# Kernel optimization log

Hardware: AMD Instinct MI355X
Metric: run time of the kernel (lower is better)

Reference implementation:

```python
import jax, jax.numpy as jnp
import numpy as np

N_ITEM_SRC = 100000
N_ITEM_DST = 50000
N_USER0 = 50000
N_USER1 = 25000
E_II = 800000
E_IU0 = 800000
E_IU1 = 400000
D_IN = 256
D_H = 256
D_OUT = 128


def setup_inputs() -> dict:
    key = jax.random.key(0)
    ks = jax.random.split(key, 16)
    f = jnp.float32
    s = 0.05  # weight init scale
    return {
        "x_item": jax.random.normal(ks[0], (N_ITEM_SRC, D_IN), f),
        "x_user": jax.random.normal(ks[1], (N_USER0, D_H), f),
        "src_ii": jax.random.randint(ks[2], (E_II,), 0, N_ITEM_SRC, jnp.int32),
        "dst_ii": jax.random.randint(ks[3], (E_II,), 0, N_ITEM_DST, jnp.int32),
        "src_iu0": jax.random.randint(ks[4], (E_IU0,), 0, N_ITEM_SRC, jnp.int32),
        "dst_iu0": jax.random.randint(ks[5], (E_IU0,), 0, N_USER0, jnp.int32),
        "src_iu1": jax.random.randint(ks[6], (E_IU1,), 0, N_ITEM_DST, jnp.int32),
        "dst_iu1": jax.random.randint(ks[7], (E_IU1,), 0, N_USER1, jnp.int32),
        "Wn1": jax.random.normal(ks[8], (D_IN, D_H), f) * s,
        "Ws1": jax.random.normal(ks[9], (D_IN, D_H), f) * s,
        "b1": jnp.zeros((D_H,), f),
        "Wn2": jax.random.normal(ks[10], (D_H, D_H), f) * s,
        "Ws2": jax.random.normal(ks[11], (D_H, D_H), f) * s,
        "b2": jnp.zeros((D_H,), f),
        "Wn3": jax.random.normal(ks[12], (D_H, D_H), f) * s,
        "Ws3": jax.random.normal(ks[13], (D_H, D_H), f) * s,
        "b3": jnp.zeros((D_H,), f),
        "Wlin": jax.random.normal(ks[14], (D_H, D_OUT), f) * s,
        "blin": jnp.zeros((D_OUT,), f),
        "n_item_dst": N_ITEM_DST,
        "n_user1": N_USER1,
    }


def _sage_mean(x_src, x_dst, src, dst, n_dst, Wn, Ws, b):
    """DGL SAGEConv('mean'): fc_self(x_dst) + fc_neigh(mean_{in-nbrs} x_src) + bias.
    Isolated dst nodes get zero neighbor contribution (clamp degree to 1)."""
    deg = jax.ops.segment_sum(jnp.ones(dst.shape, x_src.dtype), dst, num_segments=n_dst)
    agg = jax.ops.segment_sum(x_src[src], dst, num_segments=n_dst)  # [n_dst, d]
    agg = agg / jnp.maximum(deg, 1.0)[:, None]
    return x_dst @ Ws + agg @ Wn + b


def reference(x_item, x_user, src_ii, dst_ii, src_iu0, dst_iu0, src_iu1, dst_iu1,
              Wn1, Ws1, b1, Wn2, Ws2, b2, Wn3, Ws3, b3, Wlin, blin,
              n_item_dst, n_user1):
    # conv1: item->item (block: dst item feats are prefix of src item feats)
    item_x = jax.nn.relu(_sage_mean(x_item, x_item[:n_item_dst], src_ii, dst_ii,
                                    n_item_dst, Wn1, Ws1, b1))
    # conv2: item->user at hop 0
    user_x = jax.nn.relu(_sage_mean(x_item, x_user, src_iu0, dst_iu0,
                                    x_user.shape[0], Wn2, Ws2, b2))
    user_x = user_x[:n_user1]
    # conv3: item->user at hop 1
    user_x = jax.nn.relu(_sage_mean(item_x, user_x, src_iu1, dst_iu1,
                                    n_user1, Wn3, Ws3, b3))
    return user_x @ Wlin + blin
```

## Files before the change

### kernel.cpp

```cpp
#include <hip/hip_runtime.h>

#define D 256
#define NI_SRC 100000
#define NI_DST 50000
#define NU1 25000
#define EII 800000
#define EIU0 800000
#define EIU1 400000
#define DOUT 128
#define CAP 56
#define CSTRIDE 16

#define NB_BUCKET 512
#define NB_WCVT 1664
#define NB_CVT 12500
#define NGRP1 100000
#define NGRP2 100000
#define NGRP3 50000
#define NGRP 250000

typedef __bf16 bf16x8 __attribute__((ext_vector_type(8)));
typedef float f32x4 __attribute__((ext_vector_type(4)));

__device__ __forceinline__ unsigned short f2bf(float x) {
    unsigned u = __builtin_bit_cast(unsigned, x);
    u += 0x7FFFu + ((u >> 16) & 1u);
    return (unsigned short)(u >> 16);
}
__device__ __forceinline__ float bflo(unsigned u) { return __builtin_bit_cast(float, u << 16); }
__device__ __forceinline__ float bfhi(unsigned u) { return __builtin_bit_cast(float, u & 0xFFFF0000u); }

__device__ __forceinline__ void bucket8p(const int* __restrict__ src, const int* __restrict__ dst,
                                         int* __restrict__ cur, int* __restrict__ csr,
                                         int g, int dmax) {
    const int4 da = reinterpret_cast<const int4*>(dst)[g * 2];
    const int4 db = reinterpret_cast<const int4*>(dst)[g * 2 + 1];
    const int4 sa = reinterpret_cast<const int4*>(src)[g * 2];
    const int4 sb = reinterpret_cast<const int4*>(src)[g * 2 + 1];
    int d[8] = {da.x, da.y, da.z, da.w, db.x, db.y, db.z, db.w};
    int s[8] = {sa.x, sa.y, sa.z, sa.w, sb.x, sb.y, sb.z, sb.w};
    int p[8];
#pragma unroll
    for (int q = 0; q < 8; ++q)
        p[q] = (d[q] < dmax) ? atomicAdd(&cur[d[q] * CSTRIDE], 1) : CAP;
#pragma unroll
    for (int q = 0; q < 8; ++q)
        if (p[q] < CAP) csr[d[q] * CAP + p[q]] = s[q];
}

__global__ __launch_bounds__(256) void prep_kernel(
    const int* __restrict__ s1, const int* __restrict__ d1, int* __restrict__ c1, int* __restrict__ e1,
    const int* __restrict__ s2, const int* __restrict__ d2, int* __restrict__ c2, int* __restrict__ e2,
    const int* __restrict__ s3, const int* __restrict__ d3, int* __restrict__ c3, int* __restrict__ e3,
    const float* __restrict__ W0, const float* __restrict__ W1, const float* __restrict__ W2,
    const float* __restrict__ W3, const float* __restrict__ W4, const float* __restrict__ W5,
    const float* __restrict__ W6, unsigned short* __restrict__ wout,
    const float* __restrict__ xin, unsigned short* __restrict__ xout)
{
    int b = blockIdx.x;
    if (b < NB_BUCKET) {
        int t0 = b * 256 + threadIdx.x;
        for (int g = t0; g < NGRP; g += NB_BUCKET * 256) {
            if (g < NGRP1) bucket8p(s1, d1, c1, e1, g, NI_DST);
            else if (g < NGRP1 + NGRP2) bucket8p(s2, d2, c2, e2, g - NGRP1, NU1);
            else bucket8p(s3, d3, c3, e3, g - NGRP1 - NGRP2, NU1);
        }
    } else if (b < NB_BUCKET + NB_WCVT) {
        int t = (b - NB_BUCKET) * 256 + threadIdx.x;
        const float* W; int NN; int base;
        if (t < 393216) {
            int w = t >> 16; base = w << 16;
            W = (w == 0) ? W0 : (w == 1) ? W1 : (w == 2) ? W2 : (w == 3) ? W3 : (w == 4) ? W4 : W5;
            NN = 256;
        } else { base = 393216; W = W6; NN = 128; }
        int i = t - base;
        int n = i >> 8, k = i & 255;
        wout[t] = f2bf(W[(size_t)k * NN + n]);
    } else {
        long i = (long)(b - NB_BUCKET - NB_WCVT) * 256 + threadIdx.x;
        const float4 f1 = *reinterpret_cast<const float4*>(xin + i * 8);
        const float4 f2 = *reinterpret_cast<const float4*>(xin + i * 8 + 4);
        uint4 v;
        v.x = f2bf(f1.x) | ((unsigned)f2bf(f1.y) << 16);
        v.y = f2bf(f1.z) | ((unsigned)f2bf(f1.w) << 16);
        v.z = f2bf(f2.x) | ((unsigned)f2bf(f2.y) << 16);
        v.w = f2bf(f2.z) | ((unsigned)f2bf(f2.w) << 16);
        *reinterpret_cast<uint4*>(xout + i * 8) = v;
    }
}

__device__ __forceinline__ void gather_seg(const unsigned short* __restrict__ X,
                                           const int* __restrict__ csr,
                                           const int* __restrict__ cnt,
                                           unsigned short* __restrict__ out,
                                           int nrows, int wid, int lane) {
    if (wid >= nrows) return;
    int c = min(cnt[wid * CSTRIDE], CAP);
    const int len0 = (c + 1) >> 1;
    const int half = lane >> 5;
    const int l32 = lane & 31;
    const int myc = half ? (c - len0) : len0;
    int myid = (l32 < myc) ? csr[wid * CAP + half * len0 + l32] : 0;
    float acc[8] = {};
    for (int t = 0; t < len0; ++t) {
        int sid = __shfl(myid, t + half * 32, 64);
        if (t < myc) {
            const uint4 v = *reinterpret_cast<const uint4*>(X + (size_t)sid * D + l32 * 8);
            acc[0] += bflo(v.x); acc[1] += bfhi(v.x);
            acc[2] += bflo(v.y); acc[3] += bfhi(v.y);
            acc[4] += bflo(v.z); acc[5] += bfhi(v.z);
            acc[6] += bflo(v.w); acc[7] += bfhi(v.w);
        }
    }
#pragma unroll
    for (int q = 0; q < 8; ++q) acc[q] += __shfl_xor(acc[q], 32, 64);
    if (half == 0) {
        float r = 1.0f / fmaxf((float)c, 1.0f);
        uint4 o;
        o.x = f2bf(acc[0] * r) | ((unsigned)f2bf(acc[1] * r) << 16);
        o.y = f2bf(acc[2] * r) | ((unsigned)f2bf(acc[3] * r) << 16);
        o.z = f2bf(acc[4] * r) | ((unsigned)f2bf(acc[5] * r) << 16);
        o.w = f2bf(acc[6] * r) | ((unsigned)f2bf(acc[7] * r) << 16);
        *reinterpret_cast<uint4*>(out + (size_t)wid * D + l32 * 8) = o;
    }
}

__global__ __launch_bounds__(256) void gather_cap(const unsigned short* __restrict__ X,
                                                  const int* __restrict__ csr,
                                                  const int* __restrict__ cnt,
                                                  unsigned short* __restrict__ out, int nrows) {
    int wid = (blockIdx.x * blockDim.x + threadIdx.x) >> 6;
    gather_seg(X, csr, cnt, out, nrows, wid, threadIdx.x & 63);
}

__global__ __launch_bounds__(256) void gather12(const unsigned short* __restrict__ X,
                                                const int* __restrict__ csr1, const int* __restrict__ cnt1,
                                                unsigned short* __restrict__ out1,
                                                const int* __restrict__ csr2, const int* __restrict__ cnt2,
                                                unsigned short* __restrict__ out2)
{
    int wid = (blockIdx.x * blockDim.x + threadIdx.x) >> 6;
    int lane = threadIdx.x & 63;
    if (wid < NI_DST) gather_seg(X, csr1, cnt1, out1, NI_DST, wid, lane);
    else gather_seg(X, csr2, cnt2, out2, NU1, wid - NI_DST, lane);
}

template<bool A1F32, bool HAS_AGG, bool RELU, bool OUTF32>
__device__ __forceinline__ void gemm_body(
    int bx, int by, unsigned short* sA, unsigned short* sB,
    const unsigned short* __restrict__ A1b, const float* __restrict__ A1f,
    const unsigned short* __restrict__ A2,
    const unsigned short* __restrict__ W1t, const unsigned short* __restrict__ W2t,
    const float* __restrict__ bias,
    unsigned short* __restrict__ Cb, float* __restrict__ Cf,
    int M, int N)
{
    const int tid = threadIdx.x;
    const int lane = tid & 63;
    const int wid = tid >> 6;
    const int wrow = (wid >> 1) * 64;
    const int wcol = (wid & 1) * 64;
    const int brow = bx * 128;
    const int bcol = by * 128;

    f32x4 acc[4][4] = {};

    const int r0 = tid >> 2;
    const int k0 = (tid & 3) * 8;

    const int nPass = HAS_AGG ? 2 : 1;
    for (int pass = 0; pass < nPass; ++pass) {
        const unsigned short* __restrict__ Wt = pass ? W2t : W1t;
        for (int kt = 0; kt < 256; kt += 32) {
#pragma unroll
            for (int c = 0; c < 2; ++c) {
                int row = r0 + c * 64;
                int grow = brow + row;
                uint4 val = {0u, 0u, 0u, 0u};
                if (pass == 0) {
                    if (A1F32) {
                        if (grow < M) {
                            const float4 f1 = *reinterpret_cast<const float4*>(A1f + (size_t)grow * 256 + kt + k0);
                            const float4 f2 = *reinterpret_cast<const float4*>(A1f + (size_t)grow * 256 + kt + k0 + 4);
                            val.x = f2bf(f1.x) | ((unsigned)f2bf(f1.y) << 16);
                            val.y = f2bf(f1.z) | ((unsigned)f2bf(f1.w) << 16);
                            val.z = f2bf(f2.x) | ((unsigned)f2bf(f2.y) << 16);
                            val.w = f2bf(f2.z) | ((unsigned)f2bf(f2.w) << 16);
                        }
                    } else {
                        if (grow < M) val = *reinterpret_cast<const uint4*>(A1b + (size_t)grow * 256 + kt + k0);
                    }
                } else {
                    if (grow < M) val = *reinterpret_cast<const uint4*>(A2 + (size_t)grow * 256 + kt + k0);
                }
                *reinterpret_cast<uint4*>(sA + row * 40 + k0) = val;
                *reinterpret_cast<uint4*>(sB + row * 40 + k0) =
                    *reinterpret_cast<const uint4*>(Wt + (size_t)(bcol + row) * 256 + kt + k0);
            }
            __syncthreads();
            const int fr = lane & 15;
            const int fk = (lane >> 4) * 8;
            bf16x8 af[4], bfr[4];
#pragma unroll
            for (int f = 0; f < 4; ++f) {
                af[f]  = __builtin_bit_cast(bf16x8, *reinterpret_cast<const uint4*>(sA + (wrow + f * 16 + fr) * 40 + fk));
                bfr[f] = __builtin_bit_cast(bf16x8, *reinterpret_cast<const uint4*>(sB + (wcol + f * 16 + fr) * 40 + fk));
            }
#pragma unroll
            for (int mi = 0; mi < 4; ++mi)
#pragma unroll
                for (int ni = 0; ni < 4; ++ni)
                    acc[mi][ni] = __builtin_amdgcn_mfma_f32_16x16x32_bf16(af[mi], bfr[ni], acc[mi][ni], 0, 0, 0);
            __syncthreads();
        }
    }

    const int cr = (lane >> 4) * 4;
    const int cc = lane & 15;
#pragma unroll
    for (int mi = 0; mi < 4; ++mi) {
#pragma unroll
        for (int j = 0; j < 4; ++j) {
            int grow = brow + wrow + mi * 16 + cr + j;
            if (grow >= M) continue;
#pragma unroll
            for (int ni = 0; ni < 4; ++ni) {
                int gcol = bcol + wcol + ni * 16 + cc;
                float v = acc[mi][ni][j] + bias[gcol];
                if (RELU) v = fmaxf(v, 0.f);
                if (OUTF32) Cf[(size_t)grow * N + gcol] = v;
                else Cb[(size_t)grow * N + gcol] = f2bf(v);
            }
        }
    }
}

template<bool A1F32, bool HAS_AGG, bool RELU, bool OUTF32>
__global__ __launch_bounds__(256) void sage_gemm(
    const unsigned short* __restrict__ A1b, const float* __restrict__ A1f,
    const unsigned short* __restrict__ A2,
    const unsigned short* __restrict__ W1t, const unsigned short* __restrict__ W2t,
    const float* __restrict__ bias,
    unsigned short* __restrict__ Cb, float* __restrict__ Cf,
    int M, int N)
{
    __shared__ unsigned short sA[128 * 40];
    __shared__ unsigned short sB[128 * 40];
    gemm_body<A1F32, HAS_AGG, RELU, OUTF32>(blockIdx.x, blockIdx.y, sA, sB,
        A1b, A1f, A2, W1t, W2t, bias, Cb, Cf, M, N);
}

__global__ __launch_bounds__(256) void gemm12(
    const float* __restrict__ x_item, const unsigned short* __restrict__ agg1,
    const unsigned short* __restrict__ Wt_s1, const unsigned short* __restrict__ Wt_n1,
    const float* __restrict__ b1, unsigned short* __restrict__ item_x, int ng1,
    const float* __restrict__ x_user, const unsigned short* __restrict__ agg2,
    const unsigned short* __restrict__ Wt_s2, const unsigned short* __restrict__ Wt_n2,
    const float* __restrict__ b2, unsigned short* __restrict__ user_x2)
{
    __shared__ unsigned short sA[128 * 40];
    __shared__ unsigned short sB[128 * 40];
    int b = blockIdx.x;
    if (b < ng1) {
        gemm_body<true, true, true, false>(b >> 1, b & 1, sA, sB,
            nullptr, x_item, agg1, Wt_s1, Wt_n1, b1, item_x, nullptr, NI_DST, 256);
    } else {
        int b2i = b - ng1;
        gemm_body<true, true, true, false>(b2i >> 1, b2i & 1, sA, sB,
            nullptr, x_user, agg2, Wt_s2, Wt_n2, b2, user_x2, nullptr, NU1, 256);
    }
}

extern "C" void kernel_launch(void* const* d_in, const int* in_sizes, int n_in,
                              void* d_out, int out_size, void* d_ws, size_t ws_size,
                              hipStream_t stream) {
    const float* x_item = (const float*)d_in[0];
    const float* x_user = (const float*)d_in[1];
    const int* src_ii  = (const int*)d_in[2];
    const int* dst_ii  = (const int*)d_in[3];
    const int* src_iu0 = (const int*)d_in[4];
    const int* dst_iu0 = (const int*)d_in[5];
    const int* src_iu1 = (const int*)d_in[6];
    const int* dst_iu1 = (const int*)d_in[7];
    const float* Wn1 = (const float*)d_in[8];
    const float* Ws1 = (const float*)d_in[9];
    const float* b1  = (const float*)d_in[10];
    const float* Wn2 = (const float*)d_in[11];
    const float* Ws2 = (const float*)d_in[12];
    const float* b2  = (const float*)d_in[13];
    const float* Wn3 = (const float*)d_in[14];
    const float* Ws3 = (const float*)d_in[15];
    const float* b3  = (const float*)d_in[16];
    const float* Wlin = (const float*)d_in[17];
    const float* blin = (const float*)d_in[18];
    float* out = (float*)d_out;

    unsigned short* xb_item = (unsigned short*)d_ws;
    unsigned short* wts     = xb_item + 25600000;
    unsigned short* agg1    = wts + 425984;
    unsigned short* agg2    = agg1 + 12800000;
    int* cur  = (int*)(agg2 + 6400000);
    int* csr3 = cur + 1600000;
    unsigned short* item_x = (unsigned short*)(csr3 + 1400000);
    int* csr1 = (int*)item_x;
    int* csr2 = csr1 + 2800000;

    int* cur1 = cur;
    int* cur2 = cur + 50000 * CSTRIDE;
    int* cur3 = cur + 75000 * CSTRIDE;

    unsigned short* user_x2 = xb_item;
    unsigned short* agg3    = xb_item + 6400000;
    unsigned short* user_x3 = xb_item + 12800000;

    unsigned short* Wt_s1 = wts;
    unsigned short* Wt_n1 = wts + 65536;
    unsigned short* Wt_s2 = wts + 2 * 65536;
    unsigned short* Wt_n2 = wts + 3 * 65536;
    unsigned short* Wt_s3 = wts + 4 * 65536;
    unsigned short* Wt_n3 = wts + 5 * 65536;
    unsigned short* Wt_li = wts + 6 * 65536;

    hipMemsetAsync(cur, 0, sizeof(int) * 1600000, stream);

    prep_kernel<<<NB_BUCKET + NB_WCVT + NB_CVT, 256, 0, stream>>>(
        src_ii, dst_ii, cur1, csr1,
        src_iu0, dst_iu0, cur2, csr2,
        src_iu1, dst_iu1, cur3, csr3,
        Ws1, Wn1, Ws2, Wn2, Ws3, Wn3, Wlin, wts,
        x_item, xb_item);

    gather12<<<(NI_DST + NU1) * 64 / 256, 256, 0, stream>>>(
        xb_item, csr1, cur1, agg1, csr2, cur2, agg2);

    const int ng1 = ((NI_DST + 127) / 128) * 2;
    const int ng2 = ((NU1 + 127) / 128) * 2;
    gemm12<<<ng1 + ng2, 256, 0, stream>>>(
        x_item, agg1, Wt_s1, Wt_n1, b1, item_x, ng1,
        x_user, agg2, Wt_s2, Wt_n2, b2, user_x2);

    gather_cap<<<(NU1 * 64) / 256, 256, 0, stream>>>(item_x, csr3, cur3, agg3, NU1);

    dim3 g2((NU1 + 127) / 128, 2);
    sage_gemm<false, true, true, false><<<g2, 256, 0, stream>>>(
        user_x2, nullptr, agg3, Wt_s3, Wt_n3, b3, user_x3, nullptr, NU1, D);

    dim3 g4((NU1 + 127) / 128, 1);
    sage_gemm<false, false, false, true><<<g4, 256, 0, stream>>>(
        user_x3, nullptr, nullptr, Wt_li, nullptr, blin, nullptr, out, NU1, DOUT);
}
```

Before: 352.5 us.

## Co-schedule edge bucketing, gathers and GEMMs across fused kernels

```diff
diff --git a/kernel.cpp b/kernel.cpp
--- a/kernel.cpp
+++ b/kernel.cpp
@@ -9,7 +9,6 @@
 #define EIU1 400000
 #define DOUT 128
 #define CAP 56
-#define CSTRIDE 16
 
 #define NB_BUCKET 512
 #define NB_WCVT 1664
@@ -17,7 +16,6 @@
 #define NGRP1 100000
 #define NGRP2 100000
 #define NGRP3 50000
-#define NGRP 250000
 
 typedef __bf16 bf16x8 __attribute__((ext_vector_type(8)));
 typedef float f32x4 __attribute__((ext_vector_type(4)));
@@ -30,9 +28,9 @@
 __device__ __forceinline__ float bflo(unsigned u) { return __builtin_bit_cast(float, u << 16); }
 __device__ __forceinline__ float bfhi(unsigned u) { return __builtin_bit_cast(float, u & 0xFFFF0000u); }
 
-__device__ __forceinline__ void bucket8p(const int* __restrict__ src, const int* __restrict__ dst,
-                                         int* __restrict__ cur, int* __restrict__ csr,
-                                         int g, int dmax) {
+__device__ __forceinline__ void bucket8(const int* __restrict__ src, const int* __restrict__ dst,
+                                        int* __restrict__ cur, int* __restrict__ csr,
+                                        int g, int dmax) {
     const int4 da = reinterpret_cast<const int4*>(dst)[g * 2];
     const int4 db = reinterpret_cast<const int4*>(dst)[g * 2 + 1];
     const int4 sa = reinterpret_cast<const int4*>(src)[g * 2];
@@ -42,16 +40,14 @@
     int p[8];
 #pragma unroll
     for (int q = 0; q < 8; ++q)
-        p[q] = (d[q] < dmax) ? atomicAdd(&cur[d[q] * CSTRIDE], 1) : CAP;
+        p[q] = (d[q] < dmax) ? atomicAdd(&cur[d[q]], 1) : CAP;
 #pragma unroll
     for (int q = 0; q < 8; ++q)
         if (p[q] < CAP) csr[d[q] * CAP + p[q]] = s[q];
 }
 
-__global__ __launch_bounds__(256) void prep_kernel(
+__global__ __launch_bounds__(256) void prep1_kernel(
     const int* __restrict__ s1, const int* __restrict__ d1, int* __restrict__ c1, int* __restrict__ e1,
-    const int* __restrict__ s2, const int* __restrict__ d2, int* __restrict__ c2, int* __restrict__ e2,
-    const int* __restrict__ s3, const int* __restrict__ d3, int* __restrict__ c3, int* __restrict__ e3,
     const float* __restrict__ W0, const float* __restrict__ W1, const float* __restrict__ W2,
     const float* __restrict__ W3, const float* __restrict__ W4, const float* __restrict__ W5,
     const float* __restrict__ W6, unsigned short* __restrict__ wout,
@@ -60,11 +56,8 @@
     int b = blockIdx.x;
     if (b < NB_BUCKET) {
         int t0 = b * 256 + threadIdx.x;
-        for (int g = t0; g < NGRP; g += NB_BUCKET * 256) {
-            if (g < NGRP1) bucket8p(s1, d1, c1, e1, g, NI_DST);
-            else if (g < NGRP1 + NGRP2) bucket8p(s2, d2, c2, e2, g - NGRP1, NU1);
-            else bucket8p(s3, d3, c3, e3, g - NGRP1 - NGRP2, NU1);
-        }
+        for (int g = t0; g < NGRP1; g += NB_BUCKET * 256)
+            bucket8(s1, d1, c1, e1, g, NI_DST);
     } else if (b < NB_BUCKET + NB_WCVT) {
         int t = (b - NB_BUCKET) * 256 + threadIdx.x;
         const float* W; int NN; int base;
@@ -95,7 +88,7 @@
                                            unsigned short* __restrict__ out,
                                            int nrows, int wid, int lane) {
     if (wid >= nrows) return;
-    int c = min(cnt[wid * CSTRIDE], CAP);
+    int c = min(cnt[wid], CAP);
     const int len0 = (c + 1) >> 1;
     const int half = lane >> 5;
     const int l32 = lane & 31;
@@ -125,24 +118,23 @@
     }
 }
 
-__global__ __launch_bounds__(256) void gather_cap(const unsigned short* __restrict__ X,
-                                                  const int* __restrict__ csr,
-                                                  const int* __restrict__ cnt,
-                                                  unsigned short* __restrict__ out, int nrows) {
-    int wid = (blockIdx.x * blockDim.x + threadIdx.x) >> 6;
-    gather_seg(X, csr, cnt, out, nrows, wid, threadIdx.x & 63);
-}
-
-__global__ __launch_bounds__(256) void gather12(const unsigned short* __restrict__ X,
-                                                const int* __restrict__ csr1, const int* __restrict__ cnt1,
-                                                unsigned short* __restrict__ out1,
-                                                const int* __restrict__ csr2, const int* __restrict__ cnt2,
-                                                unsigned short* __restrict__ out2)
-{
-    int wid = (blockIdx.x * blockDim.x + threadIdx.x) >> 6;
-    int lane = threadIdx.x & 63;
-    if (wid < NI_DST) gather_seg(X, csr1, cnt1, out1, NI_DST, wid, lane);
-    else gather_seg(X, csr2, cnt2, out2, NU1, wid - NI_DST, lane);
+__global__ __launch_bounds__(256) void bucket23_gather1(
+    const int* __restrict__ s2, const int* __restrict__ d2, int* __restrict__ c2, int* __restrict__ e2,
+    const int* __restrict__ s3, const int* __restrict__ d3, int* __restrict__ c3, int* __restrict__ e3,
+    const unsigned short* __restrict__ X, const int* __restrict__ csr1,
+    const int* __restrict__ cnt1, unsigned short* __restrict__ out1)
+{
+    int b = blockIdx.x;
+    if (b < NB_BUCKET) {
+        int t0 = b * 256 + threadIdx.x;
+        for (int g = t0; g < NGRP2 + NGRP3; g += NB_BUCKET * 256) {
+            if (g < NGRP2) bucket8(s2, d2, c2, e2, g, NU1);
+            else bucket8(s3, d3, c3, e3, g - NGRP2, NU1);
+        }
+    } else {
+        int wid = (b - NB_BUCKET) * 4 + (threadIdx.x >> 6);
+        gather_seg(X, csr1, cnt1, out1, NI_DST, wid, threadIdx.x & 63);
+    }
 }
 
 template<bool A1F32, bool HAS_AGG, bool RELU, bool OUTF32>
@@ -250,24 +242,40 @@
         A1b, A1f, A2, W1t, W2t, bias, Cb, Cf, M, N);
 }
 
-__global__ __launch_bounds__(256) void gemm12(
-    const float* __restrict__ x_item, const unsigned short* __restrict__ agg1,
+__global__ __launch_bounds__(256) void gemm1_gather2(
+    const unsigned short* __restrict__ xb, const unsigned short* __restrict__ agg1,
     const unsigned short* __restrict__ Wt_s1, const unsigned short* __restrict__ Wt_n1,
     const float* __restrict__ b1, unsigned short* __restrict__ item_x, int ng1,
-    const float* __restrict__ x_user, const unsigned short* __restrict__ agg2,
-    const unsigned short* __restrict__ Wt_s2, const unsigned short* __restrict__ Wt_n2,
-    const float* __restrict__ b2, unsigned short* __restrict__ user_x2)
+    const int* __restrict__ csr2, const int* __restrict__ cnt2, unsigned short* __restrict__ agg2)
 {
     __shared__ unsigned short sA[128 * 40];
     __shared__ unsigned short sB[128 * 40];
     int b = blockIdx.x;
     if (b < ng1) {
+        gemm_body<false, true, true, false>(b >> 1, b & 1, sA, sB,
+            xb, nullptr, agg1, Wt_s1, Wt_n1, b1, item_x, nullptr, NI_DST, 256);
+    } else {
+        int wid = (b - ng1) * 4 + (threadIdx.x >> 6);
+        gather_seg(xb, csr2, cnt2, agg2, NU1, wid, threadIdx.x & 63);
+    }
+}
+
+__global__ __launch_bounds__(256) void gemm2_gather3(
+    const float* __restrict__ x_user, const unsigned short* __restrict__ agg2,
+    const unsigned short* __restrict__ Wt_s2, const unsigned short* __restrict__ Wt_n2,
+    const float* __restrict__ b2, unsigned short* __restrict__ user_x2, int ng2,
+    const unsigned short* __restrict__ item_x,
+    const int* __restrict__ csr3, const int* __restrict__ cnt3, unsigned short* __restrict__ agg3)
+{
+    __shared__ unsigned short sA[128 * 40];
+    __shared__ unsigned short sB[128 * 40];
+    int b = blockIdx.x;
+    if (b < ng2) {
         gemm_body<true, true, true, false>(b >> 1, b & 1, sA, sB,
-            nullptr, x_item, agg1, Wt_s1, Wt_n1, b1, item_x, nullptr, NI_DST, 256);
+            nullptr, x_user, agg2, Wt_s2, Wt_n2, b2, user_x2, nullptr, NU1, 256);
     } else {
-        int b2i = b - ng1;
-        gemm_body<true, true, true, false>(b2i >> 1, b2i & 1, sA, sB,
-            nullptr, x_user, agg2, Wt_s2, Wt_n2, b2, user_x2, nullptr, NU1, 256);
+        int wid = (b - ng2) * 4 + (threadIdx.x >> 6);
+        gather_seg(item_x, csr3, cnt3, agg3, NU1, wid, threadIdx.x & 63);
     }
 }
 
@@ -300,14 +308,14 @@
     unsigned short* agg1    = wts + 425984;
     unsigned short* agg2    = agg1 + 12800000;
     int* cur  = (int*)(agg2 + 6400000);
-    int* csr3 = cur + 1600000;
+    int* csr3 = cur + 100000;
     unsigned short* item_x = (unsigned short*)(csr3 + 1400000);
     int* csr1 = (int*)item_x;
-    int* csr2 = csr1 + 2800000;
+    int* csr2 = (int*)(item_x + 12800000);
 
     int* cur1 = cur;
-    int* cur2 = cur + 50000 * CSTRIDE;
-    int* cur3 = cur + 75000 * CSTRIDE;
+    int* cur2 = cur + 50000;
+    int* cur3 = cur + 75000;
 
     unsigned short* user_x2 = xb_item;
     unsigned short* agg3    = xb_item + 6400000;
@@ -321,25 +329,27 @@
     unsigned short* Wt_n3 = wts + 5 * 65536;
     unsigned short* Wt_li = wts + 6 * 65536;
 
-    hipMemsetAsync(cur, 0, sizeof(int) * 1600000, stream);
-
-    prep_kernel<<<NB_BUCKET + NB_WCVT + NB_CVT, 256, 0, stream>>>(
+    hipMemsetAsync(cur, 0, sizeof(int) * 100000, stream);
+
+    prep1_kernel<<<NB_BUCKET + NB_WCVT + NB_CVT, 256, 0, stream>>>(
         src_ii, dst_ii, cur1, csr1,
+        Ws1, Wn1, Ws2, Wn2, Ws3, Wn3, Wlin, wts,
+        x_item, xb_item);
+
+    bucket23_gather1<<<NB_BUCKET + NI_DST / 4, 256, 0, stream>>>(
         src_iu0, dst_iu0, cur2, csr2,
         src_iu1, dst_iu1, cur3, csr3,
-        Ws1, Wn1, Ws2, Wn2, Ws3, Wn3, Wlin, wts,
-        x_item, xb_item);
-
-    gather12<<<(NI_DST + NU1) * 64 / 256, 256, 0, stream>>>(
-        xb_item, csr1, cur1, agg1, csr2, cur2, agg2);
+        xb_item, csr1, cur1, agg1);
 
     const int ng1 = ((NI_DST + 127) / 128) * 2;
+    gemm1_gather2<<<ng1 + NU1 / 4, 256, 0, stream>>>(
+        xb_item, agg1, Wt_s1, Wt_n1, b1, item_x, ng1,
+        csr2, cur2, agg2);
+
     const int ng2 = ((NU1 + 127) / 128) * 2;
-    gemm12<<<ng1 + ng2, 256, 0, stream>>>(
-        x_item, agg1, Wt_s1, Wt_n1, b1, item_x, ng1,
-        x_user, agg2, Wt_s2, Wt_n2, b2, user_x2);
-
-    gather_cap<<<(NU1 * 64) / 256, 256, 0, stream>>>(item_x, csr3, cur3, agg3, NU1);
+    gemm2_gather3<<<ng2 + NU1 / 4, 256, 0, stream>>>(
+        x_user, agg2, Wt_s2, Wt_n2, b2, user_x2, ng2,
+        item_x, csr3, cur3, agg3);
 
     dim3 g2((NU1 + 127) / 128, 2);
     sage_gemm<false, true, true, false><<<g2, 256, 0, stream>>>(
```

Measured after the change: 348.4 us (median of 2 runs). Within noise of the previous version (-1.2%).
